# Performance work log

Hardware: AMD Instinct MI355X
Metric: run time of the kernel (lower is better)

Reference implementation:

```python
import jax, jax.numpy as jnp
import numpy as np

N, L, D = 4, 2048, 1024
H_DIM, OUT_DIM = 1024, 1024


def setup_inputs() -> dict:
    key = jax.random.key(0)
    ks = jax.random.split(key, 7)
    scale = 0.02
    return {
        "x": jax.random.normal(ks[0], (N, L, D), dtype=jnp.float32),
        "Wq": jax.random.normal(ks[1], (D, H_DIM), dtype=jnp.float32) * scale,
        "bq": jnp.zeros((H_DIM,), dtype=jnp.float32),
        "Wk": jax.random.normal(ks[2], (D, H_DIM), dtype=jnp.float32) * scale,
        "bk": jnp.zeros((H_DIM,), dtype=jnp.float32),
        "Wv": jax.random.normal(ks[3], (D, OUT_DIM), dtype=jnp.float32) * scale,
        "bv": jnp.zeros((OUT_DIM,), dtype=jnp.float32),
    }


def reference(x, Wq, bq, Wk, bk, Wv, bv):
    # q,k: [N,L,h_dim], v: [N,L,out_dim]
    q = jnp.einsum("nld,dh->nlh", x, Wq) + bq
    k = jnp.einsum("nld,dh->nlh", x, Wk) + bk
    v = jnp.einsum("nld,do->nlo", x, Wv) + bv
    # scores: [N,L,L]
    qk = jnp.einsum("nlh,nmh->nlm", q, k)
    # NOTE: original scales by sqrt(qk.shape[-1]) == sqrt(L) (seq len), not sqrt(h_dim)
    seq_len = qk.shape[-1]
    s = jax.nn.softmax(qk / jnp.sqrt(jnp.asarray(seq_len, dtype=qk.dtype)), axis=-1)
    return jnp.einsum("nlm,nmo->nlo", s, v)
```

## Files before the change

kernel.cpp:

```cpp
#include <hip/hip_runtime.h>
#include <hip/hip_bf16.h>


typedef __attribute__((ext_vector_type(8))) short bf16x8;
typedef __attribute__((ext_vector_type(4))) float f32x4;

#define AS_G(p) ((__attribute__((address_space(1))) void*)(p))
#define AS_L(p) ((__attribute__((address_space(3))) void*)(p))

__device__ __forceinline__ unsigned short f2bf(float f) {
  unsigned int u = __float_as_uint(f);
  unsigned int lsb = (u >> 16) & 1u;
  u += 0x7fffu + lsb;
  return (unsigned short)(u >> 16);
}

#define WAITV0 asm volatile("s_waitcnt vmcnt(0)" ::: "memory")
#define BARRIER() do { __builtin_amdgcn_s_barrier(); asm volatile("" ::: "memory"); } while (0)


#define STAGE_A(ktk, h, bofs) do { _Pragma("unroll")                               \
    for (int u_ = 0; u_ < 2; u_++)                                                 \
      __builtin_amdgcn_global_load_lds(                                            \
          AS_G(A + (size_t)(rowBase + (h) * 128 + u_ * 64 + r0) * lda + (ktk) + goff), \
          AS_L(lds + (bofs) + ((h) * 128 + u_ * 64) * 64 + t * 8), 16, 0, 0);      \
  } while (0)

#define STAGE_B(ktk, h, bofs) do { _Pragma("unroll")                               \
    for (int u_ = 0; u_ < 2; u_++)                                                 \
      __builtin_amdgcn_global_load_lds(                                            \
          AS_G(B + (size_t)(colBase + (h) * 128 + u_ * 64 + r0) * ldb + (ktk) + goff), \
          AS_L(lds + (bofs) + 16384 + ((h) * 128 + u_ * 64) * 64 + t * 8), 16, 0, 0); \
  } while (0)

#define LOAD_A(ih, bofs) do { _Pragma("unroll")                                    \
    for (int ks_ = 0; ks_ < 2; ks_++) { _Pragma("unroll")                          \
      for (int ii = 0; ii < 4; ii++) {                                             \
        int row_ = wrow + ((ih) * 4 + ii) * 16 + r16;                              \
        int slot_ = (ks_ * 4 + q) ^ (r16 & 7);                                     \
        af[ks_][ii] = *(const bf16x8*)(lds + (bofs) + row_ * 64 + slot_ * 8);      \
      } } } while (0)

#define LOAD_B(jh, bofs) do { _Pragma("unroll")                                    \
    for (int ks_ = 0; ks_ < 2; ks_++) { _Pragma("unroll")                          \
      for (int jj = 0; jj < 2; jj++) {                                             \
        int row_ = wcol + ((jh) * 2 + jj) * 16 + r16;                              \
        int slot_ = (ks_ * 4 + q) ^ (r16 & 7);                                     \
        bfr[ks_][(jh) * 2 + jj] =                                                  \
            *(const bf16x8*)(lds + (bofs) + 16384 + row_ * 64 + slot_ * 8);        \
      } } } while (0)

#define MM(ih, jh) do { __builtin_amdgcn_s_setprio(1); _Pragma("unroll")           \
    for (int ks_ = 0; ks_ < 2; ks_++) { _Pragma("unroll")                          \
      for (int ii = 0; ii < 4; ii++) { _Pragma("unroll")                           \
        for (int jj = 0; jj < 2; jj++)                                             \
          acc[(ih) * 4 + ii][(jh) * 2 + jj] =                                      \
              __builtin_amdgcn_mfma_f32_16x16x32_bf16(                             \
                  af[ks_][ii], bfr[ks_][(jh) * 2 + jj],                            \
                  acc[(ih) * 4 + ii][(jh) * 2 + jj], 0, 0, 0);                     \
      } }                                                                          \
    __builtin_amdgcn_s_setprio(0); } while (0)

#define KTILE(ktk, bofs, obofs, doStage) do {                                      \
                                                                 \
    LOAD_A(0, bofs); LOAD_B(0, bofs);                                              \
    if (doStage) { STAGE_B((ktk) + 64, 1, obofs); STAGE_A((ktk) + 64, 0, obofs); } \
    BARRIER(); MM(0, 0); BARRIER();                                                \
                                                                 \
    LOAD_B(1, bofs);                                                               \
    if (doStage) { STAGE_A((ktk) + 64, 1, obofs); STAGE_B((ktk) + 64, 0, obofs); } \
    BARRIER(); MM(0, 1); BARRIER();                                                \
                                                                 \
    LOAD_A(1, bofs);                                                               \
    BARRIER(); MM(1, 1); BARRIER();                                                \
                                    \
    MM(1, 0); WAITV0; BARRIER(); } while (0)

template <int EPI>
__global__ __launch_bounds__(512, 2) void gemm_8p(
    const unsigned short* __restrict__ A, const unsigned short* __restrict__ B,
    float* __restrict__ Cf, long long sA, long long sB, long long sC,
    int K, int lda, int ldb, int ldc,
    unsigned short* __restrict__ u0, unsigned short* __restrict__ u1,
    unsigned short* __restrict__ u2,
    const float* __restrict__ f0, const float* __restrict__ f1,
    const float* __restrict__ f2,
    float* __restrict__ rsum, float scale)
{
  __shared__ unsigned short lds[2 * 32768];

  const int t = threadIdx.x;
  const int rowBase = blockIdx.y * 256;
  const int colBase = blockIdx.x * 256;
  A += (long long)blockIdx.z * sA;
  B += (long long)blockIdx.z * sB;

  const int l = t & 63;
  const int w = t >> 6;
  const int wrow = (w >> 2) * 128;
  const int wcol = (w & 3) * 64;
  const int q = l >> 4;
  const int r16 = l & 15;

  const int r0 = t >> 3;
  const int goff = ((t & 7) ^ (r0 & 7)) << 3;

  f32x4 acc[8][4] = {};
  bf16x8 af[2][4], bfr[2][4];

  const int NT = K >> 6;

  STAGE_A(0, 0, 0); STAGE_A(0, 1, 0);
  STAGE_B(0, 0, 0); STAGE_B(0, 1, 0);
  WAITV0; BARRIER();

  for (int kt2 = 0; kt2 < NT; kt2 += 2) {
    KTILE(kt2 * 64, 0, 32768, true);
    KTILE(kt2 * 64 + 64, 32768, 0, kt2 + 2 < NT);
  }

  if (EPI == 1) {
    unsigned short* p16 = u0 + (long long)blockIdx.z * sC;
    float* rs = rsum + (long long)blockIdx.z * 2048;
#pragma unroll
    for (int i = 0; i < 8; i++) {
#pragma unroll
      for (int r = 0; r < 4; r++) {
        int row = rowBase + wrow + i * 16 + q * 4 + r;
        float rowpart = 0.f;
#pragma unroll
        for (int j = 0; j < 4; j++) {
          int col = colBase + wcol + j * 16 + r16;
          float e = __expf(acc[i][j][r] * scale);
          p16[(size_t)row * ldc + col] = f2bf(e);
          rowpart += e;
        }
#pragma unroll
        for (int m = 1; m < 16; m <<= 1) rowpart += __shfl_xor(rowpart, m);
        if (r16 == 0) atomicAdd(rs + row, rowpart);
      }
    }
  } else if (EPI == 2) {
    const int seg = colBase >> 10;
    if (seg < 2) {
      unsigned short* dst = seg ? u1 : u0;
      const float* bias = seg ? f1 : f0;
      const int cb = colBase & 1023;
#pragma unroll
      for (int i = 0; i < 8; i++) {
#pragma unroll
        for (int r = 0; r < 4; r++) {
          int row = rowBase + wrow + i * 16 + q * 4 + r;
#pragma unroll
          for (int j = 0; j < 4; j++) {
            int col = cb + wcol + j * 16 + r16;
            dst[(size_t)row * 1024 + col] = f2bf(acc[i][j][r] + bias[col]);
          }
        }
      }
    } else {
      const int ob = colBase - 2048;
#pragma unroll
      for (int i = 0; i < 8; i++) {
        int posBase = rowBase + wrow + i * 16 + q * 4;
        int b = posBase >> 11;
        int pos = posBase & 2047;
#pragma unroll
        for (int j = 0; j < 4; j++) {
          int o = ob + wcol + j * 16 + r16;
          float bias = f2[o];
          ushort4 pk;
          pk.x = f2bf(acc[i][j][0] + bias);
          pk.y = f2bf(acc[i][j][1] + bias);
          pk.z = f2bf(acc[i][j][2] + bias);
          pk.w = f2bf(acc[i][j][3] + bias);
          *(ushort4*)(u2 + ((size_t)((b << 10) + o) * 2048 + pos)) = pk;
        }
      }
    }
  } else {
    float* C = Cf + (long long)blockIdx.z * sC;
    const float* rs = rsum + (long long)blockIdx.z * 2048;
#pragma unroll
    for (int i = 0; i < 8; i++) {
#pragma unroll
      for (int r = 0; r < 4; r++) {
        int row = rowBase + wrow + i * 16 + q * 4 + r;
        float inv = 1.0f / rs[row];
#pragma unroll
        for (int j = 0; j < 4; j++) {
          int col = colBase + wcol + j * 16 + r16;
          C[(size_t)row * ldc + col] = acc[i][j][r] * inv;
        }
      }
    }
  }
}


__global__ __launch_bounds__(256) void cast_f32_to_bf16(
    const float* __restrict__ in, unsigned short* __restrict__ out, int n4,
    float* __restrict__ rzero, int nz4)
{
  int i = blockIdx.x * 256 + threadIdx.x;
  if (i < nz4) ((float4*)rzero)[i] = make_float4(0.f, 0.f, 0.f, 0.f);
  if (i >= n4) return;
  float4 v = ((const float4*)in)[i];
  ushort4 o;
  o.x = f2bf(v.x); o.y = f2bf(v.y); o.z = f2bf(v.z); o.w = f2bf(v.w);
  ((ushort4*)out)[i] = o;
}


__global__ __launch_bounds__(256) void wtrans(
    const float* __restrict__ Wq, const float* __restrict__ Wk,
    const float* __restrict__ Wv, unsigned short* __restrict__ WT)
{
  __shared__ float tile[32][33];
  const float* in = blockIdx.z == 0 ? Wq : (blockIdx.z == 1 ? Wk : Wv);
  unsigned short* out = WT + (size_t)blockIdx.z * 1024 * 1024;
  const int bc = blockIdx.x * 32;
  const int br = blockIdx.y * 32;
  const int tx = threadIdx.x;
  const int ty = threadIdx.y;
#pragma unroll
  for (int i = 0; i < 4; i++)
    tile[ty + i * 8][tx] = in[(size_t)(br + ty + i * 8) * 1024 + bc + tx];
  __syncthreads();
#pragma unroll
  for (int i = 0; i < 4; i++)
    out[(size_t)(bc + ty + i * 8) * 1024 + br + tx] = f2bf(tile[tx][ty + i * 8]);
}


extern "C" void kernel_launch(void* const* d_in, const int* in_sizes, int n_in,
                              void* d_out, int out_size, void* d_ws, size_t ws_size,
                              hipStream_t stream) {
  (void)in_sizes; (void)n_in; (void)out_size;

  const float* x  = (const float*)d_in[0];
  const float* Wq = (const float*)d_in[1];
  const float* bq = (const float*)d_in[2];
  const float* Wk = (const float*)d_in[3];
  const float* bk = (const float*)d_in[4];
  const float* Wv = (const float*)d_in[5];
  const float* bv = (const float*)d_in[6];
  float* out = (float*)d_out;

  const int Nb = 4, L = 2048, D = 1024, H = 1024, O = 1024;
  const int M = Nb * L;
  const int NQKV = 3 * H;

  char* ws = (char*)d_ws;
  size_t off = 0;
  unsigned short* xb = (unsigned short*)(ws + off); off += (size_t)M * D * 2;
  unsigned short* qb = (unsigned short*)(ws + off); off += (size_t)M * H * 2;
  unsigned short* kb = (unsigned short*)(ws + off); off += (size_t)M * H * 2;
  unsigned short* vt = (unsigned short*)(ws + off); off += (size_t)M * O * 2;
  unsigned short* WT = (unsigned short*)(ws + off); off += (size_t)NQKV * D * 2;
  unsigned short* P  = (unsigned short*)(ws + off); off += (size_t)Nb * L * L * 2;
  float* rsum = (float*)(ws + off); off += (size_t)Nb * L * 4;
  if (ws_size < off) return;

  dim3 blk256(256);
  dim3 blk512(512);

  cast_f32_to_bf16<<<(M * D / 4 + 255) / 256, blk256, 0, stream>>>(
      x, xb, M * D / 4, rsum, Nb * L / 4);

  wtrans<<<dim3(32, 32, 3), dim3(32, 8), 0, stream>>>(Wq, Wk, Wv, WT);

  gemm_8p<2><<<dim3(NQKV / 256, M / 256, 1), blk512, 0, stream>>>(
      xb, WT, nullptr, 0, 0, 0, D, D, D, 0,
      qb, kb, vt, bq, bk, bv, nullptr, 0.f);

  gemm_8p<1><<<dim3(L / 256, L / 256, Nb), blk512, 0, stream>>>(
      qb, kb, nullptr, (long long)L * H, (long long)L * H, (long long)L * L,
      H, H, H, L,
      P, nullptr, nullptr, nullptr, nullptr, nullptr,
      rsum, 0.022097086912079608f );

  gemm_8p<3><<<dim3(O / 256, L / 256, Nb), blk512, 0, stream>>>(
      P, vt, out, (long long)L * L, (long long)O * L, (long long)L * O,
      L, L, L, O,
      nullptr, nullptr, nullptr, nullptr, nullptr, nullptr,
      rsum, 0.f);
}
```

Baseline: 259.4 us.

## Deepen GEMM LDS prefetch to two tiles ahead with partial vmcnt waits

The GEMM main loop now stages the tile two K-steps ahead into the same LDS buffer it is consuming. Each 64-row chunk is issued once the fragments it overwrites have been read into registers. The end-of-tile wait becomes vmcnt(8) instead of vmcnt(0), so the next tile's loads can stay in flight across the barrier. This aims to hide global-load latency better, but it relies on exact ordering between the LDS fragment reads and the overwriting async loads, and it assumes K is a multiple of 128.

```diff
diff --git a/kernel.cpp b/kernel.cpp
--- a/kernel.cpp
+++ b/kernel.cpp
@@ -15,66 +15,72 @@
   return (unsigned short)(u >> 16);
 }
 
-#define WAITV0 asm volatile("s_waitcnt vmcnt(0)" ::: "memory")
+#define WAITV(n) asm volatile("s_waitcnt vmcnt(" #n ")" ::: "memory")
 #define BARRIER() do { __builtin_amdgcn_s_barrier(); asm volatile("" ::: "memory"); } while (0)
 
 
-#define STAGE_A(ktk, h, bofs) do { _Pragma("unroll")                               \
-    for (int u_ = 0; u_ < 2; u_++)                                                 \
-      __builtin_amdgcn_global_load_lds(                                            \
-          AS_G(A + (size_t)(rowBase + (h) * 128 + u_ * 64 + r0) * lda + (ktk) + goff), \
-          AS_L(lds + (bofs) + ((h) * 128 + u_ * 64) * 64 + t * 8), 16, 0, 0);      \
-  } while (0)
-
-#define STAGE_B(ktk, h, bofs) do { _Pragma("unroll")                               \
-    for (int u_ = 0; u_ < 2; u_++)                                                 \
-      __builtin_amdgcn_global_load_lds(                                            \
-          AS_G(B + (size_t)(colBase + (h) * 128 + u_ * 64 + r0) * ldb + (ktk) + goff), \
-          AS_L(lds + (bofs) + 16384 + ((h) * 128 + u_ * 64) * 64 + t * 8), 16, 0, 0); \
-  } while (0)
-
-#define LOAD_A(ih, bofs) do { _Pragma("unroll")                                    \
-    for (int ks_ = 0; ks_ < 2; ks_++) { _Pragma("unroll")                          \
-      for (int ii = 0; ii < 4; ii++) {                                             \
-        int row_ = wrow + ((ih) * 4 + ii) * 16 + r16;                              \
-        int slot_ = (ks_ * 4 + q) ^ (r16 & 7);                                     \
-        af[ks_][ii] = *(const bf16x8*)(lds + (bofs) + row_ * 64 + slot_ * 8);      \
+#define S64A(ktk, rb, bofs)                                                   \
+  __builtin_amdgcn_global_load_lds(                                           \
+      AS_G(A + (size_t)(rowBase + (rb) * 64 + r0) * lda + (ktk) + goff),      \
+      AS_L(lds + (bofs) + (rb) * 4096 + t * 8), 16, 0, 0)
+
+#define S64B(ktk, rb, bofs)                                                   \
+  __builtin_amdgcn_global_load_lds(                                           \
+      AS_G(B + (size_t)(colBase + (rb) * 64 + r0) * ldb + (ktk) + goff),      \
+      AS_L(lds + (bofs) + 16384 + (rb) * 4096 + t * 8), 16, 0, 0)
+
+#define STAGE_TILE(ktk, bofs) do {                                            \
+    S64A(ktk, 0, bofs); S64A(ktk, 1, bofs);                                   \
+    S64A(ktk, 2, bofs); S64A(ktk, 3, bofs);                                   \
+    S64B(ktk, 0, bofs); S64B(ktk, 1, bofs);                                   \
+    S64B(ktk, 2, bofs); S64B(ktk, 3, bofs); } while (0)
+
+#define LOAD_A(ih, bofs) do { _Pragma("unroll")                               \
+    for (int ks_ = 0; ks_ < 2; ks_++) { _Pragma("unroll")                     \
+      for (int ii = 0; ii < 4; ii++) {                                        \
+        int row_ = wrow + ((ih) * 4 + ii) * 16 + r16;                         \
+        int slot_ = (ks_ * 4 + q) ^ (r16 & 7);                                \
+        af[ks_][ii] = *(const bf16x8*)(lds + (bofs) + row_ * 64 + slot_ * 8); \
       } } } while (0)
 
-#define LOAD_B(jh, bofs) do { _Pragma("unroll")                                    \
-    for (int ks_ = 0; ks_ < 2; ks_++) { _Pragma("unroll")                          \
-      for (int jj = 0; jj < 2; jj++) {                                             \
-        int row_ = wcol + ((jh) * 2 + jj) * 16 + r16;                              \
-        int slot_ = (ks_ * 4 + q) ^ (r16 & 7);                                     \
-        bfr[ks_][(jh) * 2 + jj] =                                                  \
-            *(const bf16x8*)(lds + (bofs) + 16384 + row_ * 64 + slot_ * 8);        \
+#define LOAD_B(jh, bofs) do { _Pragma("unroll")                               \
+    for (int ks_ = 0; ks_ < 2; ks_++) { _Pragma("unroll")                     \
+      for (int jj = 0; jj < 2; jj++) {                                        \
+        int row_ = wcol + ((jh) * 2 + jj) * 16 + r16;                         \
+        int slot_ = (ks_ * 4 + q) ^ (r16 & 7);                                \
+        bfr[ks_][(jh) * 2 + jj] =                                             \
+            *(const bf16x8*)(lds + (bofs) + 16384 + row_ * 64 + slot_ * 8);   \
       } } } while (0)
 
-#define MM(ih, jh) do { __builtin_amdgcn_s_setprio(1); _Pragma("unroll")           \
-    for (int ks_ = 0; ks_ < 2; ks_++) { _Pragma("unroll")                          \
-      for (int ii = 0; ii < 4; ii++) { _Pragma("unroll")                           \
-        for (int jj = 0; jj < 2; jj++)                                             \
-          acc[(ih) * 4 + ii][(jh) * 2 + jj] =                                      \
-              __builtin_amdgcn_mfma_f32_16x16x32_bf16(                             \
-                  af[ks_][ii], bfr[ks_][(jh) * 2 + jj],                            \
-                  acc[(ih) * 4 + ii][(jh) * 2 + jj], 0, 0, 0);                     \
-      } }                                                                          \
+#define MM(ih, jh) do { __builtin_amdgcn_s_setprio(1); _Pragma("unroll")      \
+    for (int ks_ = 0; ks_ < 2; ks_++) { _Pragma("unroll")                     \
+      for (int ii = 0; ii < 4; ii++) { _Pragma("unroll")                      \
+        for (int jj = 0; jj < 2; jj++)                                        \
+          acc[(ih) * 4 + ii][(jh) * 2 + jj] =                                 \
+              __builtin_amdgcn_mfma_f32_16x16x32_bf16(                        \
+                  af[ks_][ii], bfr[ks_][(jh) * 2 + jj],                       \
+                  acc[(ih) * 4 + ii][(jh) * 2 + jj], 0, 0, 0);                \
+      } }                                                                     \
     __builtin_amdgcn_s_setprio(0); } while (0)
 
-#define KTILE(ktk, bofs, obofs, doStage) do {                                      \
-                                                                 \
-    LOAD_A(0, bofs); LOAD_B(0, bofs);                                              \
-    if (doStage) { STAGE_B((ktk) + 64, 1, obofs); STAGE_A((ktk) + 64, 0, obofs); } \
-    BARRIER(); MM(0, 0); BARRIER();                                                \
-                                                                 \
-    LOAD_B(1, bofs);                                                               \
-    if (doStage) { STAGE_A((ktk) + 64, 1, obofs); STAGE_B((ktk) + 64, 0, obofs); } \
-    BARRIER(); MM(0, 1); BARRIER();                                                \
-                                                                 \
-    LOAD_A(1, bofs);                                                               \
-    BARRIER(); MM(1, 1); BARRIER();                                                \
-                                    \
-    MM(1, 0); WAITV0; BARRIER(); } while (0)
+#define KTILE(ktc, bofs, ST) do {                                             \
+                                                   \
+    LOAD_A(0, bofs); LOAD_B(0, bofs);                                         \
+    BARRIER(); MM(0, 0); BARRIER();                                           \
+                            \
+    LOAD_B(1, bofs);                                                          \
+    if (ST) { S64A((ktc) + 128, 0, bofs); S64A((ktc) + 128, 2, bofs); }       \
+    BARRIER(); MM(0, 1); BARRIER();                                           \
+                            \
+    LOAD_A(1, bofs);                                                          \
+    if (ST) { S64B((ktc) + 128, 0, bofs); S64B((ktc) + 128, 1, bofs);         \
+              S64B((ktc) + 128, 2, bofs); S64B((ktc) + 128, 3, bofs); }       \
+    BARRIER(); MM(1, 1); BARRIER();                                           \
+          \
+    if (ST) { S64A((ktc) + 128, 1, bofs); S64A((ktc) + 128, 3, bofs); }       \
+    BARRIER(); MM(1, 0);                                                      \
+    if (ST) { WAITV(8); } else { WAITV(0); }                                  \
+    BARRIER(); } while (0)
 
 template <int EPI>
 __global__ __launch_bounds__(512, 2) void gemm_8p(
@@ -108,16 +114,18 @@
   f32x4 acc[8][4] = {};
   bf16x8 af[2][4], bfr[2][4];
 
-  const int NT = K >> 6;
-
-  STAGE_A(0, 0, 0); STAGE_A(0, 1, 0);
-  STAGE_B(0, 0, 0); STAGE_B(0, 1, 0);
-  WAITV0; BARRIER();
-
-  for (int kt2 = 0; kt2 < NT; kt2 += 2) {
-    KTILE(kt2 * 64, 0, 32768, true);
-    KTILE(kt2 * 64 + 64, 32768, 0, kt2 + 2 < NT);
+  STAGE_TILE(0, 0);
+  STAGE_TILE(64, 32768);
+  WAITV(8);
+  BARRIER();
+
+  int kt = 0;
+  for (; kt + 128 < K; kt += 128) {
+    KTILE(kt, 0, 1);
+    KTILE(kt + 64, 32768, 1);
   }
+  KTILE(kt, 0, 0);
+  KTILE(kt + 64, 32768, 0);
 
   if (EPI == 1) {
     unsigned short* p16 = u0 + (long long)blockIdx.z * sC;
```

After: 256.4 us. About the same (-1.2%).
